# Performance work log

Measured on AMD Instinct MI355X. Metric: run time of the kernel, lower is better.

## Reference

```python
import jax, jax.numpy as jnp
import numpy as np

D_MODEL = 1024
N_HEADS = 16
HEAD_DIM = D_MODEL // N_HEADS
ROPE_BASE = 10000.0


def _rope_cos_sin(t, dtype):
    # inv_freq over half the head dim, standard RoPE (GPT-NeoX style)
    inv_freq = 1.0 / (ROPE_BASE ** (jnp.arange(0, HEAD_DIM, 2, dtype=jnp.float32) / HEAD_DIM))
    freqs = jnp.arange(t, dtype=jnp.float32)[:, None] * inv_freq[None, :]  # [t, hd/2]
    emb = jnp.concatenate([freqs, freqs], axis=-1)  # [t, hd]
    return jnp.cos(emb).astype(dtype), jnp.sin(emb).astype(dtype)


def _rotate_half(x):
    x1, x2 = jnp.split(x, 2, axis=-1)
    return jnp.concatenate([-x2, x1], axis=-1)


def _apply_rope(x, cos, sin):
    # x: [b, h, t, hd]; cos/sin: [t, hd]
    return x * cos[None, None] + _rotate_half(x) * sin[None, None]


def setup_inputs() -> dict:
    key = jax.random.key(0)
    kx, kqkv, kout = jax.random.split(key, 3)
    x = jax.random.normal(kx, (4, 2048, D_MODEL), dtype=jnp.float32)
    scale = 1.0 / np.sqrt(D_MODEL)
    Wqkv = jax.random.normal(kqkv, (D_MODEL, 3 * D_MODEL), dtype=jnp.float32) * scale
    Wout = jax.random.normal(kout, (D_MODEL, D_MODEL), dtype=jnp.float32) * scale
    return {"x": x, "Wqkv": Wqkv, "Wout": Wout}


def reference(x, Wqkv, Wout):
    b, t, _ = x.shape
    qkv = (x @ Wqkv).reshape(b, t, 3, N_HEADS, HEAD_DIM)
    q, k, v = qkv[:, :, 0], qkv[:, :, 1], qkv[:, :, 2]  # [b, t, h, hd]
    q = q.transpose(0, 2, 1, 3)  # [b, h, t, hd]
    k = k.transpose(0, 2, 1, 3)
    v = v.transpose(0, 2, 1, 3)
    cos, sin = _rope_cos_sin(t, x.dtype)
    q = _apply_rope(q, cos, sin)
    k = _apply_rope(k, cos, sin)
    # causal SDPA
    scores = jnp.einsum("bhqd,bhkd->bhqk", q, k) / np.sqrt(HEAD_DIM)
    causal = jnp.tril(jnp.ones((t, t), dtype=bool))
    scores = jnp.where(causal[None, None], scores, jnp.finfo(scores.dtype).min)
    attn = jax.nn.softmax(scores, axis=-1)
    out = jnp.einsum("bhqk,bhkd->bhqd", attn, v)
    out = out.transpose(0, 2, 1, 3).reshape(b, t, D_MODEL)
    return out @ Wout
```

## Files before the change

kernel.cpp:

```cpp
#include <hip/hip_runtime.h>
#include <cstdint>
#include <cstddef>

typedef __bf16 bf16;
typedef __bf16 bf16x8 __attribute__((ext_vector_type(8)));
typedef __bf16 bf16x4 __attribute__((ext_vector_type(4)));
typedef __bf16 bf16x2 __attribute__((ext_vector_type(2)));
typedef float  f32x4  __attribute__((ext_vector_type(4)));
typedef float  f32x16 __attribute__((ext_vector_type(16)));

#define MFMA16(a, b, c) __builtin_amdgcn_mfma_f32_16x16x32_bf16((a), (b), (c), 0, 0, 0)
#define MFMA32(a, b, c) __builtin_amdgcn_mfma_f32_32x32x16_bf16((a), (b), (c), 0, 0, 0)

static constexpr int BB   = 4;
static constexpr int TT   = 2048;
static constexpr int DM   = 1024;
static constexpr int NH   = 16;
static constexpr int HD   = 64;
static constexpr int TOK  = BB * TT;
static constexpr int NQKV = 3 * DM;

__device__ inline void gload16(const void* g, void* l) {
    __builtin_amdgcn_global_load_lds((const __attribute__((address_space(1))) void*)g,
                                     (__attribute__((address_space(3))) void*)l, 16, 0, 0);
}

__device__ inline int swz(int x) { return x ^ ((x >> 3) & 0x70); }

__device__ inline int pk2(float a, float b) {
    bf16x2 t; t[0] = (bf16)a; t[1] = (bf16)b;
    return __builtin_bit_cast(int, t);
}

__global__ void k_cvt(const float* __restrict__ in, bf16* __restrict__ out, int n) {
    int i = (blockIdx.x * blockDim.x + threadIdx.x) * 4;
    if (i >= n) return;
    float4 v = *(const float4*)(in + i);
    bf16x4 o;
    o[0] = (bf16)v.x; o[1] = (bf16)v.y; o[2] = (bf16)v.z; o[3] = (bf16)v.w;
    *(bf16x4*)(out + i) = o;
}

__global__ void k_transpose_cvt(const float* __restrict__ in, bf16* __restrict__ out,
                                int R, int C) {
    __shared__ bf16 tl[64 * 72];
    int tid = threadIdx.x;
    int c0 = blockIdx.x * 64, r0 = blockIdx.y * 64;
#pragma unroll
    for (int rep = 0; rep < 4; rep++) {
        int r = rep * 16 + (tid >> 4);
        int c = (tid & 15) * 4;
        float4 v = *(const float4*)(in + (size_t)(r0 + r) * C + c0 + c);
        tl[r * 72 + c + 0] = (bf16)v.x;
        tl[r * 72 + c + 1] = (bf16)v.y;
        tl[r * 72 + c + 2] = (bf16)v.z;
        tl[r * 72 + c + 3] = (bf16)v.w;
    }
    __syncthreads();
#pragma unroll
    for (int rep = 0; rep < 4; rep++) {
        int cc = rep * 16 + (tid >> 4);
        int rr = (tid & 15) * 4;
        bf16x4 o;
        o[0] = tl[(rr + 0) * 72 + cc];
        o[1] = tl[(rr + 1) * 72 + cc];
        o[2] = tl[(rr + 2) * 72 + cc];
        o[3] = tl[(rr + 3) * 72 + cc];
        *(bf16x4*)(out + (size_t)(c0 + cc) * R + r0 + rr) = o;
    }
}

__global__ void k_rope_tab(float* __restrict__ ct, float* __restrict__ st) {
    int i = blockIdx.x * blockDim.x + threadIdx.x;
    int t = i >> 5, j = i & 31;
    float invf = powf(10000.0f, -(float)j * (1.0f / 32.0f));
    float a = (float)t * invf;
    ct[i] = cosf(a);
    st[i] = sinf(a);
}

template <int MODE>
__global__ __launch_bounds__(256) void k_gemm_bt(
    const bf16* __restrict__ A, const bf16* __restrict__ Bt,
    int M, int N, int K,
    float* __restrict__ outF,
    bf16* __restrict__ qbuf, bf16* __restrict__ kbuf, bf16* __restrict__ vbuf,
    const float* __restrict__ ct, const float* __restrict__ st, float qscale) {
    __shared__ bf16 lA[2][128 * 64];
    __shared__ bf16 lB[2][128 * 64];
    int tid = threadIdx.x;
    int l = tid & 63, wid = tid >> 6;
    int wm = wid >> 1, wn = wid & 1;
    int bn = blockIdx.x, bm = blockIdx.y;
    const char* AbB = (const char*)(A + (size_t)bm * 128 * K);
    const char* BbB = (const char*)(Bt + (size_t)bn * 128 * K);
    const size_t KB = (size_t)K * 2;
    f32x4 acc[4][4] = {};

#define GSTAGE(nb, kt) do {                                                                \
    _Pragma("unroll") for (int i = 0; i < 4; i++) {                                        \
        int cb = (wid * 4 + i) * 1024;               \
        int Xs = swz(cb + l * 16);                   \
        gload16(AbB + (size_t)(Xs >> 7) * KB + (size_t)(kt) * 2 + (Xs & 127),              \
                (char*)lA[nb] + cb);                                                       \
        gload16(BbB + (size_t)(Xs >> 7) * KB + (size_t)(kt) * 2 + (Xs & 127),              \
                (char*)lB[nb] + cb);                                                       \
    }                                                                                      \
} while (0)

    GSTAGE(0, 0);
    __syncthreads();
    int cur = 0;
    int nsteps = K >> 6;
    for (int t = 0; t < nsteps; t++) {
        if (t + 1 < nsteps) GSTAGE(cur ^ 1, (t + 1) << 6);
#pragma unroll
        for (int kk = 0; kk < 2; kk++) {
            bf16x8 af[4], bfr[4];
#pragma unroll
            for (int mi = 0; mi < 4; mi++) {
                int rr = wm * 64 + mi * 16 + (l & 15);
                int L = rr * 128 + (kk * 32 + (l >> 4) * 8) * 2;
                af[mi] = *(const bf16x8*)((const char*)lA[cur] + swz(L));
            }
#pragma unroll
            for (int ni = 0; ni < 4; ni++) {
                int rr = wn * 64 + ni * 16 + (l & 15);
                int L = rr * 128 + (kk * 32 + (l >> 4) * 8) * 2;
                bfr[ni] = *(const bf16x8*)((const char*)lB[cur] + swz(L));
            }
#pragma unroll
            for (int mi = 0; mi < 4; mi++)
#pragma unroll
                for (int ni = 0; ni < 4; ni++)
                    acc[mi][ni] = MFMA16(af[mi], bfr[ni], acc[mi][ni]);
        }
        __syncthreads();
        cur ^= 1;
    }
#undef GSTAGE

    if (MODE == 2) {
#pragma unroll
        for (int mi = 0; mi < 4; mi++) {
            int m0 = bm * 128 + wm * 64 + mi * 16 + ((l >> 4) << 2);
#pragma unroll
            for (int ni = 0; ni < 4; ni++) {
                int n = bn * 128 + wn * 64 + ni * 16 + (l & 15);
#pragma unroll
                for (int rj = 0; rj < 4; rj++)
                    outF[(size_t)(m0 + rj) * N + n] = acc[mi][ni][rj];
            }
        }
    } else {
        int n0 = bn * 128 + wn * 64;
        int sQ = n0 >> 10;
        int h = (n0 & 1023) >> 6;
        if (sQ == 2) {
#pragma unroll
            for (int ni = 0; ni < 4; ni++) {
                int d = ni * 16 + (l & 15);
#pragma unroll
                for (int mi = 0; mi < 4; mi++) {
                    int m0 = bm * 128 + wm * 64 + mi * 16 + ((l >> 4) << 2);
                    int b = m0 >> 11, t0 = m0 & 2047;
                    bf16x4 pv;
#pragma unroll
                    for (int rj = 0; rj < 4; rj++) pv[rj] = (bf16)acc[mi][ni][rj];
                    *(bf16x4*)(vbuf + ((size_t)((b * NH + h) * HD + d)) * TT + t0) = pv;
                }
            }
        } else {
            float qs = (sQ == 0) ? qscale : 1.0f;
            bf16* obuf = (sQ == 0) ? qbuf : kbuf;
#pragma unroll
            for (int mi = 0; mi < 4; mi++) {
                int m0 = bm * 128 + wm * 64 + mi * 16 + ((l >> 4) << 2);
                int b = m0 >> 11, t0 = m0 & 2047;
#pragma unroll
                for (int rj = 0; rj < 4; rj++) {
                    int t = t0 + rj;
                    bf16* dst = obuf + ((size_t)(b * NH + h) * TT + t) * HD;
                    const float* crow = ct + t * 32;
                    const float* srow = st + t * 32;
#pragma unroll
                    for (int ni2 = 0; ni2 < 2; ni2++) {
                        int d = ni2 * 16 + (l & 15);
                        float cs = crow[d], sn = srow[d];
                        float a  = acc[mi][ni2][rj];
                        float b2 = acc[mi][ni2 + 2][rj];
                        dst[d]      = (bf16)(qs * (a  * cs - b2 * sn));
                        dst[d + 32] = (bf16)(qs * (b2 * cs + a  * sn));
                    }
                }
            }
        }
    }
}

__global__ __launch_bounds__(256, 2) void k_attn(
    const bf16* __restrict__ Q, const bf16* __restrict__ K,
    const bf16* __restrict__ Vt, bf16* __restrict__ O) {
    __shared__ bf16 lK[2][4096];
    __shared__ bf16 lV[2][4096];
    __shared__ bf16 lP[8192];
    int tid = threadIdx.x;
    int l = tid & 63, w = tid >> 6;
    int bx = blockIdx.x, by = blockIdx.y;
    int bh = bx * 8 + (by >> 3);
    int p = by & 7;
    const char* KbB = (const char*)(K + (size_t)bh * TT * HD);
    const char* VbB = (const char*)(Vt + (size_t)bh * HD * TT);
    int b = bh >> 4, h = bh & 15;

    bf16x8 ones;
#pragma unroll
    for (int e = 0; e < 8; e++) ones[e] = (bf16)1.0f;

    int prow = w * 32 + (l & 31);
    int pwbase = prow * 128;
    int pswzk = (prow & 7) << 4;
    int cbase = (l >> 5) * 8;

#define STAGE_KV(nb, j) do {                                                               \
    int X0_ = w * 1024 + l * 16;                                                           \
    const char* Kj_ = KbB + (size_t)(j) * 8192;                                            \
    gload16(Kj_ + swz(X0_),        (char*)lK[nb] + w * 1024);                              \
    gload16(Kj_ + swz(X0_ + 4096), (char*)lK[nb] + w * 1024 + 4096);                       \
    int o0_ = swz(X0_), o1_ = swz(X0_ + 4096);                                             \
    gload16(VbB + (size_t)(o0_ >> 7) * (TT * 2) + (size_t)(j) * 128 + (o0_ & 127),         \
            (char*)lV[nb] + w * 1024);                                                     \
    gload16(VbB + (size_t)(o1_ >> 7) * (TT * 2) + (size_t)(j) * 128 + (o1_ & 127),         \
            (char*)lV[nb] + w * 1024 + 4096);                                              \
} while (0)

    for (int half = 0; half < 2; half++) {
        int s = (half == 0) ? (15 - p) : p;
        int r0 = s * 128;
        int nblk = 2 * s + 2;
        int wrow = r0 + w * 32;
        const bf16* Qb = Q + ((size_t)bh * TT + wrow) * HD;
        bf16x8 qa[4];
#pragma unroll
        for (int kc = 0; kc < 4; kc++)
            qa[kc] = *(const bf16x8*)(Qb + (size_t)(l & 31) * HD + kc * 16 + (l >> 5) * 8);

        f32x16 oacc[2] = {};
        f32x16 lacc = {};

        STAGE_KV(0, 0);
        __syncthreads();
        int cur = 0;
        for (int j = 0; j < nblk; j++) {
            if (j + 1 < nblk) STAGE_KV(cur ^ 1, j + 1);
            if (j * 64 <= wrow + 31) {
                f32x16 sc[2];
#pragma unroll
                for (int r = 0; r < 16; r++) { sc[0][r] = -16.0f; sc[1][r] = -16.0f; }
                __builtin_amdgcn_s_setprio(1);
#pragma unroll
                for (int kc = 0; kc < 4; kc++)
#pragma unroll
                    for (int nj = 0; nj < 2; nj++) {
                        int rr = nj * 32 + (l & 31);
                        int L = rr * 128 + ((kc * 16 + (l >> 5) * 8) * 2 ^ ((rr & 7) << 4));
                        bf16x8 kb = *(const bf16x8*)((const char*)lK[cur] + L);
                        sc[nj] = MFMA32(kb, qa[kc], sc[nj]);
                    }
                __builtin_amdgcn_s_setprio(0);
                if (j * 64 + 63 > wrow) {
                    int q = wrow + (l & 31);
#pragma unroll
                    for (int nj = 0; nj < 2; nj++)
#pragma unroll
                        for (int r = 0; r < 16; r++) {
                            int kvg = j * 64 + nj * 32 + (r & 3) + 8 * (r >> 2) + 4 * (l >> 5);
                            if (kvg > q) sc[nj][r] = -1e30f;
                        }
                }
#pragma unroll
                for (int nj = 0; nj < 2; nj++)
#pragma unroll
                    for (int r = 0; r < 16; r++)
                        sc[nj][r] = exp2f(sc[nj][r]);
#pragma unroll
                for (int nj = 0; nj < 2; nj++)
#pragma unroll
                    for (int qd = 0; qd < 4; qd++) {
                        int2 v2;
                        v2.x = pk2(sc[nj][qd * 4 + 0], sc[nj][qd * 4 + 1]);
                        v2.y = pk2(sc[nj][qd * 4 + 2], sc[nj][qd * 4 + 3]);
                        int col2 = nj * 64 + qd * 16 + cbase;
                        *(int2*)((char*)lP + pwbase + (col2 ^ pswzk)) = v2;
                    }
                __builtin_amdgcn_s_setprio(1);
#pragma unroll
                for (int kc = 0; kc < 4; kc++) {
                    bf16x8 pa = *(const bf16x8*)((const char*)lP + pwbase
                                 + ((kc * 32 + (l >> 5) * 16) ^ pswzk));
                    lacc = MFMA32(pa, ones, lacc);
#pragma unroll
                    for (int dt = 0; dt < 2; dt++) {
                        int dd = dt * 32 + (l & 31);
                        int L = dd * 128 + ((kc * 16 + (l >> 5) * 8) * 2 ^ ((dd & 7) << 4));
                        bf16x8 vbf = *(const bf16x8*)((const char*)lV[cur] + L);
                        oacc[dt] = MFMA32(pa, vbf, oacc[dt]);
                    }
                }
                __builtin_amdgcn_s_setprio(0);
            }
            __syncthreads();
            cur ^= 1;
        }
#pragma unroll
        for (int r = 0; r < 16; r++) {
            int rq = (r & 3) + 8 * (r >> 2) + 4 * (l >> 5);
            int t = wrow + rq;
            float inv = 1.0f / lacc[r];
            size_t base = ((size_t)b * TT + t) * DM + h * HD;
#pragma unroll
            for (int dt = 0; dt < 2; dt++)
                O[base + dt * 32 + (l & 31)] = (bf16)(oacc[dt][r] * inv);
        }
    }
#undef STAGE_KV
}

extern "C" void kernel_launch(void* const* d_in, const int* in_sizes, int n_in,
                              void* d_out, int out_size, void* d_ws, size_t ws_size,
                              hipStream_t stream) {
    const float* x    = (const float*)d_in[0];
    const float* Wqkv = (const float*)d_in[1];
    const float* Wout = (const float*)d_in[2];
    float* out = (float*)d_out;

    char* ws = (char*)d_ws;
    size_t off = 0;
    auto alloc = [&](size_t bytes) {
        void* p = ws + off;
        off += (bytes + 255) & ~(size_t)255;
        return p;
    };
    bf16* xb    = (bf16*)alloc((size_t)TOK * DM * 2);
    bf16* wqkvt = (bf16*)alloc((size_t)NQKV * DM * 2);
    bf16* woutt = (bf16*)alloc((size_t)DM * DM * 2);
    bf16* qr    = (bf16*)alloc((size_t)TOK * DM * 2);
    bf16* kr    = (bf16*)alloc((size_t)TOK * DM * 2);
    bf16* vt    = (bf16*)alloc((size_t)TOK * DM * 2);
    bf16* ob    = (bf16*)alloc((size_t)TOK * DM * 2);
    float* ct   = (float*)alloc((size_t)TT * 32 * 4);
    float* st   = (float*)alloc((size_t)TT * 32 * 4);
    (void)ws_size; (void)in_sizes; (void)n_in; (void)out_size;

    k_cvt<<<TOK * DM / 4 / 256, 256, 0, stream>>>(x, xb, TOK * DM);
    k_transpose_cvt<<<dim3(NQKV / 64, DM / 64), 256, 0, stream>>>(Wqkv, wqkvt, DM, NQKV);
    k_transpose_cvt<<<dim3(DM / 64, DM / 64), 256, 0, stream>>>(Wout, woutt, DM, DM);
    k_rope_tab<<<TT * 32 / 256, 256, 0, stream>>>(ct, st);
    k_gemm_bt<1><<<dim3(NQKV / 128, TOK / 128), 256, 0, stream>>>(
        xb, wqkvt, TOK, NQKV, DM, nullptr, qr, kr, vt,
        ct, st, 0.125f * 1.4426950408889634f);
    k_attn<<<dim3(8, 64), 256, 0, stream>>>(qr, kr, vt, ob);
    k_gemm_bt<2><<<dim3(DM / 128, TOK / 128), 256, 0, stream>>>(
        ob, woutt, TOK, DM, DM, out, nullptr, nullptr, nullptr,
        nullptr, nullptr, 0.0f);
}
```

Before: 185.7 us.

## Split attention into one query tile per block and load V directly from global

The attention kernel no longer pairs a long and a short causal query tile in one block. It launches one block per 128-row query tile, doubling the grid, and orders tiles longest-first so the scheduler can balance the work. V is also no longer staged into shared memory. Each wave reads its V fragments straight from global memory into registers, which cuts LDS use and may raise occupancy, but the global loads are not prefetched and may add latency.

```diff
diff --git a/kernel.cpp b/kernel.cpp
--- a/kernel.cpp
+++ b/kernel.cpp
@@ -202,15 +202,14 @@
     const bf16* __restrict__ Q, const bf16* __restrict__ K,
     const bf16* __restrict__ Vt, bf16* __restrict__ O) {
     __shared__ bf16 lK[2][4096];
-    __shared__ bf16 lV[2][4096];
     __shared__ bf16 lP[8192];
     int tid = threadIdx.x;
     int l = tid & 63, w = tid >> 6;
     int bx = blockIdx.x, by = blockIdx.y;
-    int bh = bx * 8 + (by >> 3);
-    int p = by & 7;
+    int bh = bx * 8 + (by >> 4);
+    int s = 15 - (by & 15);
     const char* KbB = (const char*)(K + (size_t)bh * TT * HD);
-    const char* VbB = (const char*)(Vt + (size_t)bh * HD * TT);
+    const bf16* Vb = Vt + (size_t)bh * HD * TT;
     int b = bh >> 4, h = bh & 15;
 
     bf16x8 ones;
@@ -222,108 +221,103 @@
     int pswzk = (prow & 7) << 4;
     int cbase = (l >> 5) * 8;
 
-#define STAGE_KV(nb, j) do {                                                               \
+#define STAGE_K(nb, j) do {                                                                \
     int X0_ = w * 1024 + l * 16;                                                           \
     const char* Kj_ = KbB + (size_t)(j) * 8192;                                            \
     gload16(Kj_ + swz(X0_),        (char*)lK[nb] + w * 1024);                              \
     gload16(Kj_ + swz(X0_ + 4096), (char*)lK[nb] + w * 1024 + 4096);                       \
-    int o0_ = swz(X0_), o1_ = swz(X0_ + 4096);                                             \
-    gload16(VbB + (size_t)(o0_ >> 7) * (TT * 2) + (size_t)(j) * 128 + (o0_ & 127),         \
-            (char*)lV[nb] + w * 1024);                                                     \
-    gload16(VbB + (size_t)(o1_ >> 7) * (TT * 2) + (size_t)(j) * 128 + (o1_ & 127),         \
-            (char*)lV[nb] + w * 1024 + 4096);                                              \
 } while (0)
 
-    for (int half = 0; half < 2; half++) {
-        int s = (half == 0) ? (15 - p) : p;
-        int r0 = s * 128;
-        int nblk = 2 * s + 2;
-        int wrow = r0 + w * 32;
-        const bf16* Qb = Q + ((size_t)bh * TT + wrow) * HD;
-        bf16x8 qa[4];
-#pragma unroll
-        for (int kc = 0; kc < 4; kc++)
-            qa[kc] = *(const bf16x8*)(Qb + (size_t)(l & 31) * HD + kc * 16 + (l >> 5) * 8);
-
-        f32x16 oacc[2] = {};
-        f32x16 lacc = {};
-
-        STAGE_KV(0, 0);
+    int r0 = s * 128;
+    int nblk = 2 * s + 2;
+    int wrow = r0 + w * 32;
+    const bf16* Qb = Q + ((size_t)bh * TT + wrow) * HD;
+    bf16x8 qa[4];
+#pragma unroll
+    for (int kc = 0; kc < 4; kc++)
+        qa[kc] = *(const bf16x8*)(Qb + (size_t)(l & 31) * HD + kc * 16 + (l >> 5) * 8);
+
+    f32x16 oacc[2] = {};
+    f32x16 lacc = {};
+
+    STAGE_K(0, 0);
+    __syncthreads();
+    int cur = 0;
+    for (int j = 0; j < nblk; j++) {
+        if (j + 1 < nblk) STAGE_K(cur ^ 1, j + 1);
+        if (j * 64 <= wrow + 31) {
+            f32x16 sc[2];
+#pragma unroll
+            for (int r = 0; r < 16; r++) { sc[0][r] = -16.0f; sc[1][r] = -16.0f; }
+            __builtin_amdgcn_s_setprio(1);
+#pragma unroll
+            for (int kc = 0; kc < 4; kc++)
+#pragma unroll
+                for (int nj = 0; nj < 2; nj++) {
+                    int rr = nj * 32 + (l & 31);
+                    int L = rr * 128 + ((kc * 16 + (l >> 5) * 8) * 2 ^ ((rr & 7) << 4));
+                    bf16x8 kb = *(const bf16x8*)((const char*)lK[cur] + L);
+                    sc[nj] = MFMA32(kb, qa[kc], sc[nj]);
+                }
+            __builtin_amdgcn_s_setprio(0);
+            if (j * 64 + 63 > wrow) {
+                int q = wrow + (l & 31);
+#pragma unroll
+                for (int nj = 0; nj < 2; nj++)
+#pragma unroll
+                    for (int r = 0; r < 16; r++) {
+                        int kvg = j * 64 + nj * 32 + (r & 3) + 8 * (r >> 2) + 4 * (l >> 5);
+                        if (kvg > q) sc[nj][r] = -1e30f;
+                    }
+            }
+#pragma unroll
+            for (int nj = 0; nj < 2; nj++)
+#pragma unroll
+                for (int r = 0; r < 16; r++)
+                    sc[nj][r] = exp2f(sc[nj][r]);
+#pragma unroll
+            for (int nj = 0; nj < 2; nj++)
+#pragma unroll
+                for (int qd = 0; qd < 4; qd++) {
+                    int2 v2;
+                    v2.x = pk2(sc[nj][qd * 4 + 0], sc[nj][qd * 4 + 1]);
+                    v2.y = pk2(sc[nj][qd * 4 + 2], sc[nj][qd * 4 + 3]);
+                    int col2 = nj * 64 + qd * 16 + cbase;
+                    *(int2*)((char*)lP + pwbase + (col2 ^ pswzk)) = v2;
+                }
+            bf16x8 vb[4][2];
+#pragma unroll
+            for (int kc = 0; kc < 4; kc++)
+#pragma unroll
+                for (int dt = 0; dt < 2; dt++)
+                    vb[kc][dt] = *(const bf16x8*)(Vb + (size_t)(dt * 32 + (l & 31)) * TT
+                                                  + j * 64 + kc * 16 + (l >> 5) * 8);
+            __builtin_amdgcn_s_setprio(1);
+#pragma unroll
+            for (int kc = 0; kc < 4; kc++) {
+                bf16x8 pa = *(const bf16x8*)((const char*)lP + pwbase
+                             + ((kc * 32 + (l >> 5) * 16) ^ pswzk));
+                lacc = MFMA32(pa, ones, lacc);
+#pragma unroll
+                for (int dt = 0; dt < 2; dt++)
+                    oacc[dt] = MFMA32(pa, vb[kc][dt], oacc[dt]);
+            }
+            __builtin_amdgcn_s_setprio(0);
+        }
         __syncthreads();
-        int cur = 0;
-        for (int j = 0; j < nblk; j++) {
-            if (j + 1 < nblk) STAGE_KV(cur ^ 1, j + 1);
-            if (j * 64 <= wrow + 31) {
-                f32x16 sc[2];
-#pragma unroll
-                for (int r = 0; r < 16; r++) { sc[0][r] = -16.0f; sc[1][r] = -16.0f; }
-                __builtin_amdgcn_s_setprio(1);
-#pragma unroll
-                for (int kc = 0; kc < 4; kc++)
-#pragma unroll
-                    for (int nj = 0; nj < 2; nj++) {
-                        int rr = nj * 32 + (l & 31);
-                        int L = rr * 128 + ((kc * 16 + (l >> 5) * 8) * 2 ^ ((rr & 7) << 4));
-                        bf16x8 kb = *(const bf16x8*)((const char*)lK[cur] + L);
-                        sc[nj] = MFMA32(kb, qa[kc], sc[nj]);
-                    }
-                __builtin_amdgcn_s_setprio(0);
-                if (j * 64 + 63 > wrow) {
-                    int q = wrow + (l & 31);
-#pragma unroll
-                    for (int nj = 0; nj < 2; nj++)
-#pragma unroll
-                        for (int r = 0; r < 16; r++) {
-                            int kvg = j * 64 + nj * 32 + (r & 3) + 8 * (r >> 2) + 4 * (l >> 5);
-                            if (kvg > q) sc[nj][r] = -1e30f;
-                        }
-                }
-#pragma unroll
-                for (int nj = 0; nj < 2; nj++)
-#pragma unroll
-                    for (int r = 0; r < 16; r++)
-                        sc[nj][r] = exp2f(sc[nj][r]);
-#pragma unroll
-                for (int nj = 0; nj < 2; nj++)
-#pragma unroll
-                    for (int qd = 0; qd < 4; qd++) {
-                        int2 v2;
-                        v2.x = pk2(sc[nj][qd * 4 + 0], sc[nj][qd * 4 + 1]);
-                        v2.y = pk2(sc[nj][qd * 4 + 2], sc[nj][qd * 4 + 3]);
-                        int col2 = nj * 64 + qd * 16 + cbase;
-                        *(int2*)((char*)lP + pwbase + (col2 ^ pswzk)) = v2;
-                    }
-                __builtin_amdgcn_s_setprio(1);
-#pragma unroll
-                for (int kc = 0; kc < 4; kc++) {
-                    bf16x8 pa = *(const bf16x8*)((const char*)lP + pwbase
-                                 + ((kc * 32 + (l >> 5) * 16) ^ pswzk));
-                    lacc = MFMA32(pa, ones, lacc);
-#pragma unroll
-                    for (int dt = 0; dt < 2; dt++) {
-                        int dd = dt * 32 + (l & 31);
-                        int L = dd * 128 + ((kc * 16 + (l >> 5) * 8) * 2 ^ ((dd & 7) << 4));
-                        bf16x8 vbf = *(const bf16x8*)((const char*)lV[cur] + L);
-                        oacc[dt] = MFMA32(pa, vbf, oacc[dt]);
-                    }
-                }
-                __builtin_amdgcn_s_setprio(0);
-            }
-            __syncthreads();
-            cur ^= 1;
-        }
-#pragma unroll
-        for (int r = 0; r < 16; r++) {
-            int rq = (r & 3) + 8 * (r >> 2) + 4 * (l >> 5);
-            int t = wrow + rq;
-            float inv = 1.0f / lacc[r];
-            size_t base = ((size_t)b * TT + t) * DM + h * HD;
-#pragma unroll
-            for (int dt = 0; dt < 2; dt++)
-                O[base + dt * 32 + (l & 31)] = (bf16)(oacc[dt][r] * inv);
-        }
-    }
-#undef STAGE_KV
+        cur ^= 1;
+    }
+#pragma unroll
+    for (int r = 0; r < 16; r++) {
+        int rq = (r & 3) + 8 * (r >> 2) + 4 * (l >> 5);
+        int t = wrow + rq;
+        float inv = 1.0f / lacc[r];
+        size_t base = ((size_t)b * TT + t) * DM + h * HD;
+#pragma unroll
+        for (int dt = 0; dt < 2; dt++)
+            O[base + dt * 32 + (l & 31)] = (bf16)(oacc[dt][r] * inv);
+    }
+#undef STAGE_K
 }
 
 extern "C" void kernel_launch(void* const* d_in, const int* in_sizes, int n_in,
@@ -359,7 +353,7 @@
     k_gemm_bt<1><<<dim3(NQKV / 128, TOK / 128), 256, 0, stream>>>(
         xb, wqkvt, TOK, NQKV, DM, nullptr, qr, kr, vt,
         ct, st, 0.125f * 1.4426950408889634f);
-    k_attn<<<dim3(8, 64), 256, 0, stream>>>(qr, kr, vt, ob);
+    k_attn<<<dim3(8, 128), 256, 0, stream>>>(qr, kr, vt, ob);
     k_gemm_bt<2><<<dim3(DM / 128, TOK / 128), 256, 0, stream>>>(
         ob, woutt, TOK, DM, DM, out, nullptr, nullptr, nullptr,
         nullptr, nullptr, 0.0f);
```

Result: slower. 241.2 us (+29.9%).
